# Optimization experiments

Hardware: AMD Instinct MI355X
Metric: run time of the kernel (lower is better)

## Reference

```python
import jax, jax.numpy as jnp
import numpy as np

N_NODES = 20000


def _gcn_conv(x, edge_index, W, b):
    """PyG GCNConv: add self-loops, symmetric normalization, x @ W, scatter-add, + bias."""
    n = x.shape[0]
    loops = jnp.arange(n, dtype=edge_index.dtype)
    src = jnp.concatenate([edge_index[0], loops])  # [E+N]
    dst = jnp.concatenate([edge_index[1], loops])  # [E+N]
    # degree of target nodes (edge weight 1), self-loops guarantee deg >= 1
    deg = jax.ops.segment_sum(jnp.ones_like(dst, dtype=x.dtype), dst, num_segments=n)
    dinv = jax.lax.rsqrt(deg)
    norm = dinv[src] * dinv[dst]  # [E+N]
    h = x @ W  # [n, out] dense GEMM before aggregation (standard GCNConv ordering)
    msg = h[src] * norm[:, None]  # gather + scale over edges
    out = jax.ops.segment_sum(msg, dst, num_segments=n)  # scatter-add to targets
    return out + b


def setup_inputs() -> dict:
    key = jax.random.key(0)
    k = jax.random.split(key, 6)
    in_f, h_f, n_cls = 512, 512, 256
    x = jax.random.normal(k[0], (N_NODES, in_f), dtype=jnp.float32)
    edge_index = jax.random.randint(k[1], (2, 160000), 0, N_NODES, dtype=jnp.int64)
    W1 = jax.random.normal(k[2], (in_f, h_f), dtype=jnp.float32) * (1.0 / np.sqrt(in_f))
    b1 = jnp.zeros((h_f,), dtype=jnp.float32)
    W2 = jax.random.normal(k[3], (h_f, n_cls), dtype=jnp.float32) * (1.0 / np.sqrt(h_f))
    b2 = jnp.zeros((n_cls,), dtype=jnp.float32)
    return {"x": x, "edge_index": edge_index, "W1": W1, "b1": b1, "W2": W2, "b2": b2}


def reference(x, edge_index, W1, b1, W2, b2):
    h = jax.nn.relu(_gcn_conv(x, edge_index, W1, b1))
    h = jax.nn.relu(_gcn_conv(h, edge_index, W2, b2))
    # F.dropout in eval mode is identity; reference is deterministic eval-mode forward
    return h
```

## Files before the change

kernel.cpp:

```cpp
#include <hip/hip_runtime.h>


typedef __bf16 bf16x8 __attribute__((ext_vector_type(8)));
typedef float floatx4 __attribute__((ext_vector_type(4)));
typedef unsigned short ushort_t;
typedef unsigned int uint_t;

#define MAXD 32
#define CAP 40

__device__ inline ushort_t f2bf(float f) {
    unsigned u = __builtin_bit_cast(unsigned, f);
    unsigned r = (u + 0x7FFFu + ((u >> 16) & 1u)) >> 16;
    return (ushort_t)r;
}
__device__ inline float bf_lo(uint_t u) { return __builtin_bit_cast(float, u << 16); }
__device__ inline float bf_hi(uint_t u) { return __builtin_bit_cast(float, u & 0xFFFF0000u); }
__device__ inline uint_t pk2(float lo, float hi) {
    return (uint_t)f2bf(lo) | ((uint_t)f2bf(hi) << 16);
}

__device__ inline void transpose_tile(const float* __restrict__ in,
                                      ushort_t* __restrict__ out,
                                      int K, int N, int k0, int n0,
                                      ushort_t (*tile)[33]) {
    int tx = threadIdx.x & 31, ty = threadIdx.x >> 5;
    for (int r = ty; r < 32; r += 8)
        tile[r][tx] = f2bf(in[(size_t)(k0 + r) * N + n0 + tx]);
    __syncthreads();
    for (int r = ty; r < 32; r += 8)
        out[(size_t)(n0 + r) * K + k0 + tx] = tile[tx][r];
}

__global__ __launch_bounds__(256) void prep_fused(
    const int* __restrict__ src, const int* __restrict__ dst,
    int* __restrict__ deg, int* __restrict__ col_ell,
    int* __restrict__ ovf_cnt, int* __restrict__ ovf, int e, int nb_e,
    const float* __restrict__ x, ushort_t* __restrict__ xb, long xcount, int nb_conv,
    const float* __restrict__ W1, ushort_t* __restrict__ w1t,
    const float* __restrict__ W2, ushort_t* __restrict__ w2t) {
    __shared__ ushort_t tile[32][33];
    int b = blockIdx.x;
    if (b < nb_e) {
        int i = b * 256 + threadIdx.x;
        if (i < e) {
            int s = src[i], d = dst[i];
            int slot = atomicAdd(&deg[d], 1);
            if (slot < MAXD) {
                col_ell[d * MAXD + slot] = s;
            } else {
                int k = atomicAdd(ovf_cnt, 1);
                ovf[2 * k] = d;
                ovf[2 * k + 1] = s;
            }
        }
        return;
    }
    b -= nb_e;
    if (b < nb_conv) {
        long i = ((long)b * 256 + threadIdx.x) * 4;
        if (i < xcount) {
            float4 v = *(const float4*)(x + i);
            ushort4 o = make_ushort4(f2bf(v.x), f2bf(v.y), f2bf(v.z), f2bf(v.w));
            *(ushort4*)(xb + i) = o;
        }
        return;
    }
    b -= nb_conv;
    if (b < 256) {
        transpose_tile(W1, w1t, 512, 512, (b >> 4) * 32, (b & 15) * 32, tile);
        return;
    }
    b -= 256;
    transpose_tile(W2, w2t, 512, 256, (b >> 3) * 32, (b & 7) * 32, tile);
}

__global__ __launch_bounds__(256) void gemm_mfma(
    const ushort_t* __restrict__ A, const ushort_t* __restrict__ BT,
    ushort_t* __restrict__ C,
    int M, int N, int K, int nbx, int gemm_blocks,
    const int* __restrict__ deg, float* __restrict__ dinv_out, int n) {
    __shared__ __align__(16) ushort_t As[8192];
    __shared__ __align__(16) ushort_t Bs[8192];

    if ((int)blockIdx.x >= gemm_blocks) {
        int i = ((int)blockIdx.x - gemm_blocks) * 256 + threadIdx.x;
        if (i < n) dinv_out[i] = 1.0f / sqrtf((float)(deg[i] + 1));
        return;
    }

    const int bx = (int)blockIdx.x % nbx, by = (int)blockIdx.x / nbx;
    const int tid = threadIdx.x;
    const int w = tid >> 6, lane = tid & 63;
    const int q = lane >> 4, ml = lane & 15;
    const int wm = (w >> 1) * 64, wn = (w & 1) * 64;
    const int row0 = by * 128, col0 = bx * 128;

    const int rr = lane >> 3;
    const int gsw = (lane & 7) ^ (rr & 7);
    const ushort_t* ga[4];
    const ushort_t* gb[4];
    ushort_t* la[4];
    ushort_t* lb[4];
#pragma unroll
    for (int rp = 0; rp < 4; rp++) {
        int r = rp * 32 + w * 8 + rr;
        int gra = min(row0 + r, M - 1);
        ga[rp] = A + (size_t)gra * K + gsw * 8;
        gb[rp] = BT + (size_t)(col0 + r) * K + gsw * 8;
        la[rp] = As + rp * 2048 + w * 512;
        lb[rp] = Bs + rp * 2048 + w * 512;
    }

    const int sel = ml & 7;
    int aoff[2][4], boff[2][4];
#pragma unroll
    for (int st = 0; st < 2; st++)
#pragma unroll
        for (int i = 0; i < 4; i++) {
            int g = q + st * 4;
            aoff[st][i] = (wm + i * 16 + ml) * 64 + ((g ^ sel) << 3);
            boff[st][i] = (wn + i * 16 + ml) * 64 + ((g ^ sel) << 3);
        }

    floatx4 acc[4][4];
#pragma unroll
    for (int i = 0; i < 4; i++)
#pragma unroll
        for (int j = 0; j < 4; j++) acc[i][j] = (floatx4)0.0f;

    for (int kt = 0; kt < K; kt += 64) {
#pragma unroll
        for (int rp = 0; rp < 4; rp++) {
            __builtin_amdgcn_global_load_lds(
                (const __attribute__((address_space(1))) unsigned*)ga[rp],
                (__attribute__((address_space(3))) unsigned*)la[rp], 16, 0, 0);
            __builtin_amdgcn_global_load_lds(
                (const __attribute__((address_space(1))) unsigned*)gb[rp],
                (__attribute__((address_space(3))) unsigned*)lb[rp], 16, 0, 0);
            ga[rp] += 64; gb[rp] += 64;
        }
        __syncthreads();
#pragma unroll
        for (int st = 0; st < 2; st++) {
            bf16x8 af[4], bfr[4];
#pragma unroll
            for (int i = 0; i < 4; i++) {
                af[i] = *(const bf16x8*)(As + aoff[st][i]);
                bfr[i] = *(const bf16x8*)(Bs + boff[st][i]);
            }
#pragma unroll
            for (int i = 0; i < 4; i++)
#pragma unroll
                for (int j = 0; j < 4; j++)
                    acc[i][j] = __builtin_amdgcn_mfma_f32_16x16x32_bf16(
                        af[i], bfr[j], acc[i][j], 0, 0, 0);
        }
        __syncthreads();
    }

#pragma unroll
    for (int i = 0; i < 4; i++) {
        int rbase = row0 + wm + i * 16 + q * 4;
#pragma unroll
        for (int j = 0; j < 4; j++) {
            int gc = col0 + wn + j * 16 + ml;
#pragma unroll
            for (int r = 0; r < 4; r++) {
                int gr = rbase + r;
                if (gr < M) C[(size_t)gr * N + gc] = f2bf(acc[i][j][r]);
            }
        }
    }
}

__global__ __launch_bounds__(256) void agg1gemm2(
    const ushort_t* __restrict__ g,
    const ushort_t* __restrict__ BT,
    const int* __restrict__ deg, const int* __restrict__ col_ell,
    const int* __restrict__ ovf_cnt, const int* __restrict__ ovf,
    const float* __restrict__ dinv, const float* __restrict__ b1,
    ushort_t* __restrict__ g2, int M) {
    __shared__ __align__(16) ushort_t As[16 * 64];
    __shared__ __align__(16) ushort_t Bs[256 * 64];
    __shared__ int2  adj_s[16][CAP];
    __shared__ float b1_s[512];
    __shared__ int   cnt_s[16];

    const int tid = threadIdx.x;
    const int w = tid >> 6, lane = tid & 63;
    const int q = lane >> 4, ml = lane & 15;
    const int wn = w * 64;
    const int row0 = (int)blockIdx.x * 16;

    for (int i = tid; i < 512; i += 256) b1_s[i] = b1[i];
    {
        int r = tid >> 4, jj = tid & 15;
        int rg = min(row0 + r, M - 1);
        int cnt = min(deg[rg], MAXD);
        const int* cm = col_ell + (size_t)rg * MAXD;
#pragma unroll
        for (int pass = 0; pass < 3; pass++) {
            int j = jj + pass * 16;
            if (j >= CAP) break;
            int2 a;
            if (j == 0) {
                a.x = rg;
                a.y = __builtin_bit_cast(int, dinv[rg]);
                cnt_s[r] = cnt + 1;
            } else {
                bool vld = (j - 1) < cnt;
                int c = vld ? cm[j - 1] : rg;
                a.x = c;
                a.y = vld ? __builtin_bit_cast(int, dinv[c]) : 0;
            }
            adj_s[r][j] = a;
        }
    }
    const int nov = *ovf_cnt;

    const int rr = lane >> 3;
    const int gsw = (lane & 7) ^ (rr & 7);
    const ushort_t* gb[8];
    ushort_t* lb[8];
#pragma unroll
    for (int rp = 0; rp < 8; rp++) {
        gb[rp] = BT + (size_t)(rp * 32 + w * 8 + rr) * 512 + gsw * 8;
        lb[rp] = Bs + rp * 2048 + w * 512;
    }

    const int sel = ml & 7;
    int aoff[2], boff[2][4];
#pragma unroll
    for (int st = 0; st < 2; st++) {
        int gg = q + st * 4;
        aoff[st] = ml * 64 + ((gg ^ sel) << 3);
#pragma unroll
        for (int i = 0; i < 4; i++)
            boff[st][i] = (wn + i * 16 + ml) * 64 + ((gg ^ sel) << 3);
    }

    floatx4 acc[4];
#pragma unroll
    for (int j = 0; j < 4; j++) acc[j] = (floatx4)0.0f;

    const int gr_ = tid >> 4;
    const int fc = tid & 15;

    __syncthreads();
    const int cntR = cnt_s[gr_];
    const float pdr = __builtin_bit_cast(float, adj_s[gr_][0].y);
    const int selfR = adj_s[gr_][0].x;

    for (int kt = 0; kt < 512; kt += 64) {
#pragma unroll
        for (int rp = 0; rp < 8; rp++) {
            __builtin_amdgcn_global_load_lds(
                (const __attribute__((address_space(1))) unsigned*)gb[rp],
                (__attribute__((address_space(3))) unsigned*)lb[rp], 16, 0, 0);
            gb[rp] += 64;
        }

        const ushort_t* gk = g + kt + fc * 4;
        float a0 = 0.0f, a1 = 0.0f, a2 = 0.0f, a3 = 0.0f;
        for (int e0 = 0; e0 < cntR; e0 += 8) {
            uint2 u[8];
            float ps[8];
#pragma unroll
            for (int j = 0; j < 8; j++) {
                int2 cp = adj_s[gr_][e0 + j];
                ps[j] = __builtin_bit_cast(float, cp.y);
                u[j] = *(const uint2*)(gk + (size_t)cp.x * 512);
            }
#pragma unroll
            for (int j = 0; j < 8; j++) {
                a0 = fmaf(ps[j], bf_lo(u[j].x), a0);
                a1 = fmaf(ps[j], bf_hi(u[j].x), a1);
                a2 = fmaf(ps[j], bf_lo(u[j].y), a2);
                a3 = fmaf(ps[j], bf_hi(u[j].y), a3);
            }
        }
        for (int k2 = 0; k2 < nov; k2++) {
            if (ovf[2 * k2] == selfR) {
                int s = ovf[2 * k2 + 1];
                float ps = dinv[s];
                uint2 u = *(const uint2*)(gk + (size_t)s * 512);
                a0 = fmaf(ps, bf_lo(u.x), a0);
                a1 = fmaf(ps, bf_hi(u.x), a1);
                a2 = fmaf(ps, bf_lo(u.y), a2);
                a3 = fmaf(ps, bf_hi(u.y), a3);
            }
        }
        float4 bv = *(const float4*)(b1_s + kt + fc * 4);
        float h0 = fmaxf(fmaf(pdr, a0, bv.x), 0.0f);
        float h1 = fmaxf(fmaf(pdr, a1, bv.y), 0.0f);
        float h2 = fmaxf(fmaf(pdr, a2, bv.z), 0.0f);
        float h3 = fmaxf(fmaf(pdr, a3, bv.w), 0.0f);
        uint2 U;
        U.x = pk2(h0, h1);
        U.y = pk2(h2, h3);
        *(uint2*)(As + gr_ * 64 + (((fc >> 1) ^ (gr_ & 7)) << 3) + (fc & 1) * 4) = U;

        __syncthreads();

#pragma unroll
        for (int st = 0; st < 2; st++) {
            bf16x8 af = *(const bf16x8*)(As + aoff[st]);
#pragma unroll
            for (int j = 0; j < 4; j++) {
                bf16x8 bfr = *(const bf16x8*)(Bs + boff[st][j]);
                acc[j] = __builtin_amdgcn_mfma_f32_16x16x32_bf16(af, bfr, acc[j],
                                                                 0, 0, 0);
            }
        }
        __syncthreads();
    }

#pragma unroll
    for (int j = 0; j < 4; j++) {
        int gc = wn + j * 16 + ml;
#pragma unroll
        for (int r = 0; r < 4; r++) {
            int lrow = q * 4 + r;
            int grow = row0 + lrow;
            if (grow < M) {
                float pd = __builtin_bit_cast(float, adj_s[lrow][0].y);
                g2[(size_t)grow * 256 + gc] = f2bf(pd * acc[j][r]);
            }
        }
    }
}

__global__ __launch_bounds__(64) void aggregate2(const uint2* __restrict__ g,
                                                 const int* __restrict__ deg,
                                                 const int* __restrict__ col_ell,
                                                 const int* __restrict__ ovf_cnt,
                                                 const int* __restrict__ ovf,
                                                 const float* __restrict__ dinv,
                                                 const float* __restrict__ bias,
                                                 float* __restrict__ out) {
    const int d = blockIdx.x, t = threadIdx.x;
    const int cnt = min(deg[d], MAXD);
    const float pd = dinv[d];
    const size_t base = (size_t)d * 64 + t;
    const int* cm = col_ell + (size_t)d * MAXD;

    int cv = 0;
    float wv = 0.0f;
    if (t < MAXD && t < cnt) {
        cv = cm[t];
        wv = 1.0f;
    }
    float4 b = *(const float4*)(bias + t * 4);

    uint2 us = g[base];
    float a0 = bf_lo(us.x), a1 = bf_hi(us.x);
    float a2 = bf_lo(us.y), a3 = bf_hi(us.y);

    for (int e0 = 0; e0 < cnt; e0 += 8) {
        uint2 u[8];
        float ws[8];
#pragma unroll
        for (int j = 0; j < 8; j++) {
            int s = __shfl(cv, e0 + j);
            ws[j] = __shfl(wv, e0 + j);
            u[j] = g[(size_t)s * 64 + t];
        }
#pragma unroll
        for (int j = 0; j < 8; j++) {
            a0 = fmaf(ws[j], bf_lo(u[j].x), a0);
            a1 = fmaf(ws[j], bf_hi(u[j].x), a1);
            a2 = fmaf(ws[j], bf_lo(u[j].y), a2);
            a3 = fmaf(ws[j], bf_hi(u[j].y), a3);
        }
    }
    int nov = *ovf_cnt;
    for (int k = 0; k < nov; k++) {
        if (ovf[2 * k] == d) {
            uint2 u = g[(size_t)ovf[2 * k + 1] * 64 + t];
            a0 += bf_lo(u.x); a1 += bf_hi(u.x);
            a2 += bf_lo(u.y); a3 += bf_hi(u.y);
        }
    }
    float4 o;
    o.x = fmaxf(fmaf(pd, a0, b.x), 0.0f);
    o.y = fmaxf(fmaf(pd, a1, b.y), 0.0f);
    o.z = fmaxf(fmaf(pd, a2, b.z), 0.0f);
    o.w = fmaxf(fmaf(pd, a3, b.w), 0.0f);
    *(float4*)(out + (size_t)d * 256 + t * 4) = o;
}

extern "C" void kernel_launch(void* const* d_in, const int* in_sizes, int n_in,
                              void* d_out, int out_size, void* d_ws, size_t ws_size,
                              hipStream_t stream) {
    const float* x  = (const float*)d_in[0];
    const int*   ei = (const int*)d_in[1];
    const float* W1 = (const float*)d_in[2];
    const float* b1 = (const float*)d_in[3];
    const float* W2 = (const float*)d_in[4];
    const float* b2 = (const float*)d_in[5];
    float* out = (float*)d_out;

    const int FIN = 512, FH = 512, FOUT = 256;
    const int n = in_sizes[0] / FIN;
    const int e = in_sizes[1] / 2;
    const int* src = ei;
    const int* dst = ei + e;

    auto align_up = [](size_t v) { return (v + 255) & ~(size_t)255; };
    char* w = (char*)d_ws;
    int*      deg     = (int*)w;
    int*      ovf_cnt = deg + n;
    w += align_up((size_t)(n + 1) * 4);
    float*    dinv    = (float*)w;    w += align_up((size_t)n * 4);
    int*      col_ell = (int*)w;      w += align_up((size_t)n * MAXD * 4);
    int*      ovf     = (int*)w;      w += align_up((size_t)2048 * 4);
    ushort_t* xb      = (ushort_t*)w; w += align_up((size_t)n * FIN * 2);
    ushort_t* w1t     = (ushort_t*)w; w += align_up((size_t)FH * FIN * 2);
    ushort_t* w2t     = (ushort_t*)w; w += align_up((size_t)FOUT * FH * 2);
    ushort_t* g       = (ushort_t*)w; w += align_up((size_t)n * FH * 2);
    ushort_t* g2      = (ushort_t*)w; w += align_up((size_t)n * FOUT * 2);

    const int nb_n = (n + 255) / 256;
    const int nb_e = (e + 255) / 256;
    const long xcount = (long)n * FIN;
    const int nb_conv = (int)((xcount / 4 + 255) / 256);

    hipMemsetAsync(deg, 0, (size_t)(n + 1) * 4, stream);

    prep_fused<<<nb_e + nb_conv + 256 + 128, 256, 0, stream>>>(
        src, dst, deg, col_ell, ovf_cnt, ovf, e, nb_e,
        x, xb, xcount, nb_conv, W1, w1t, W2, w2t);

    {
        const int mb = (n + 127) / 128;
        int gemm_blocks = (FH / 128) * mb;
        gemm_mfma<<<gemm_blocks + nb_n, 256, 0, stream>>>(
            xb, w1t, g, n, FH, FIN, FH / 128, gemm_blocks, deg, dinv, n);
    }
    agg1gemm2<<<(n + 15) / 16, 256, 0, stream>>>(
        g, w2t, deg, col_ell, ovf_cnt, ovf, dinv, b1, g2, n);

    aggregate2<<<n, 64, 0, stream>>>((const uint2*)g2, deg, col_ell, ovf_cnt,
                                     ovf, dinv, b2, out);

    (void)ws_size; (void)n_in; (void)out_size;
}
```

Before: 190.6 us.

## Gather full aggregated rows once into LDS before the second-layer GEMM

The fused aggregate+GEMM kernel now handles 32 rows per 512-thread block. Each thread gathers a contiguous 32-element slice of each neighbour's row with 16-byte loads, two edges at a time. The whole 32x512 aggregated, biased and ReLU'd tile is staged in LDS before the MFMA k-loop. This replaces the earlier scheme, which gathered 4 elements per k-tile, 8 edges at a time, inside the GEMM loop. The goal is wider, more coalesced gather traffic and fewer per-tile barriers, at the cost of much more LDS per block, which limits occupancy, and less overlap between the gather and the B-tile loads.

```diff
diff --git a/kernel.cpp b/kernel.cpp
--- a/kernel.cpp
+++ b/kernel.cpp
@@ -7,7 +7,7 @@
 typedef unsigned int uint_t;
 
 #define MAXD 32
-#define CAP 40
+#define CAP 34
 
 __device__ inline ushort_t f2bf(float f) {
     unsigned u = __builtin_bit_cast(unsigned, f);
@@ -174,26 +174,26 @@
     }
 }
 
-__global__ __launch_bounds__(256) void agg1gemm2(
+__global__ __launch_bounds__(512, 4) void agg1gemm2(
     const ushort_t* __restrict__ g,
     const ushort_t* __restrict__ BT,
     const int* __restrict__ deg, const int* __restrict__ col_ell,
     const int* __restrict__ ovf_cnt, const int* __restrict__ ovf,
     const float* __restrict__ dinv, const float* __restrict__ b1,
     ushort_t* __restrict__ g2, int M) {
-    __shared__ __align__(16) ushort_t As[16 * 64];
+    __shared__ __align__(16) ushort_t As[32 * 512];
     __shared__ __align__(16) ushort_t Bs[256 * 64];
-    __shared__ int2  adj_s[16][CAP];
+    __shared__ int2  adj_s[32][CAP];
     __shared__ float b1_s[512];
-    __shared__ int   cnt_s[16];
+    __shared__ int   cnt_s[32];
 
     const int tid = threadIdx.x;
     const int w = tid >> 6, lane = tid & 63;
     const int q = lane >> 4, ml = lane & 15;
-    const int wn = w * 64;
-    const int row0 = (int)blockIdx.x * 16;
-
-    for (int i = tid; i < 512; i += 256) b1_s[i] = b1[i];
+    const int wm = (w >> 2) * 16, wn = (w & 3) * 64;
+    const int row0 = (int)blockIdx.x * 32;
+
+    b1_s[tid] = b1[tid];
     {
         int r = tid >> 4, jj = tid & 15;
         int rg = min(row0 + r, M - 1);
@@ -218,114 +218,159 @@
         }
     }
     const int nov = *ovf_cnt;
+    __syncthreads();
 
     const int rr = lane >> 3;
     const int gsw = (lane & 7) ^ (rr & 7);
-    const ushort_t* gb[8];
-    ushort_t* lb[8];
-#pragma unroll
-    for (int rp = 0; rp < 8; rp++) {
-        gb[rp] = BT + (size_t)(rp * 32 + w * 8 + rr) * 512 + gsw * 8;
-        lb[rp] = Bs + rp * 2048 + w * 512;
-    }
-
-    const int sel = ml & 7;
-    int aoff[2], boff[2][4];
-#pragma unroll
-    for (int st = 0; st < 2; st++) {
-        int gg = q + st * 4;
-        aoff[st] = ml * 64 + ((gg ^ sel) << 3);
-#pragma unroll
-        for (int i = 0; i < 4; i++)
-            boff[st][i] = (wn + i * 16 + ml) * 64 + ((gg ^ sel) << 3);
-    }
-
-    floatx4 acc[4];
-#pragma unroll
-    for (int j = 0; j < 4; j++) acc[j] = (floatx4)0.0f;
-
-    const int gr_ = tid >> 4;
-    const int fc = tid & 15;
-
-    __syncthreads();
-    const int cntR = cnt_s[gr_];
-    const float pdr = __builtin_bit_cast(float, adj_s[gr_][0].y);
-    const int selfR = adj_s[gr_][0].x;
-
-    for (int kt = 0; kt < 512; kt += 64) {
-#pragma unroll
-        for (int rp = 0; rp < 8; rp++) {
-            __builtin_amdgcn_global_load_lds(
-                (const __attribute__((address_space(1))) unsigned*)gb[rp],
-                (__attribute__((address_space(3))) unsigned*)lb[rp], 16, 0, 0);
-            gb[rp] += 64;
-        }
-
-        const ushort_t* gk = g + kt + fc * 4;
-        float a0 = 0.0f, a1 = 0.0f, a2 = 0.0f, a3 = 0.0f;
-        for (int e0 = 0; e0 < cntR; e0 += 8) {
-            uint2 u[8];
-            float ps[8];
-#pragma unroll
-            for (int j = 0; j < 8; j++) {
-                int2 cp = adj_s[gr_][e0 + j];
-                ps[j] = __builtin_bit_cast(float, cp.y);
-                u[j] = *(const uint2*)(gk + (size_t)cp.x * 512);
-            }
-#pragma unroll
-            for (int j = 0; j < 8; j++) {
-                a0 = fmaf(ps[j], bf_lo(u[j].x), a0);
-                a1 = fmaf(ps[j], bf_hi(u[j].x), a1);
-                a2 = fmaf(ps[j], bf_lo(u[j].y), a2);
-                a3 = fmaf(ps[j], bf_hi(u[j].y), a3);
-            }
-        }
-        for (int k2 = 0; k2 < nov; k2++) {
-            if (ovf[2 * k2] == selfR) {
-                int s = ovf[2 * k2 + 1];
-                float ps = dinv[s];
-                uint2 u = *(const uint2*)(gk + (size_t)s * 512);
-                a0 = fmaf(ps, bf_lo(u.x), a0);
-                a1 = fmaf(ps, bf_hi(u.x), a1);
-                a2 = fmaf(ps, bf_lo(u.y), a2);
-                a3 = fmaf(ps, bf_hi(u.y), a3);
-            }
-        }
-        float4 bv = *(const float4*)(b1_s + kt + fc * 4);
-        float h0 = fmaxf(fmaf(pdr, a0, bv.x), 0.0f);
-        float h1 = fmaxf(fmaf(pdr, a1, bv.y), 0.0f);
-        float h2 = fmaxf(fmaf(pdr, a2, bv.z), 0.0f);
-        float h3 = fmaxf(fmaf(pdr, a3, bv.w), 0.0f);
-        uint2 U;
+    const ushort_t* gb[4];
+    ushort_t* lb[4];
+#pragma unroll
+    for (int rp = 0; rp < 4; rp++) {
+        gb[rp] = BT + (size_t)(rp * 64 + w * 8 + rr) * 512 + gsw * 8;
+        lb[rp] = Bs + (rp * 64 + w * 8) * 64;
+    }
+#pragma unroll
+    for (int rp = 0; rp < 4; rp++) {
+        __builtin_amdgcn_global_load_lds(
+            (const __attribute__((address_space(1))) unsigned*)gb[rp],
+            (__attribute__((address_space(3))) unsigned*)lb[rp], 16, 0, 0);
+        gb[rp] += 64;
+    }
+
+    const int r = tid >> 4;
+    const int c = tid & 15;
+    const int cntR = cnt_s[r];
+    const float pdr = __builtin_bit_cast(float, adj_s[r][0].y);
+    const int selfR = adj_s[r][0].x;
+
+    float acc[32];
+#pragma unroll
+    for (int i = 0; i < 32; i++) acc[i] = 0.0f;
+
+    for (int e0 = 0; e0 < cntR; e0 += 2) {
+        int2 cp0 = adj_s[r][e0];
+        int2 cp1 = adj_s[r][e0 + 1];
+        float ps0 = __builtin_bit_cast(float, cp0.y);
+        float ps1 = __builtin_bit_cast(float, cp1.y);
+        const ushort_t* p0 = g + (size_t)cp0.x * 512 + c * 32;
+        const ushort_t* p1 = g + (size_t)cp1.x * 512 + c * 32;
+        uint4 u0[4], u1[4];
+#pragma unroll
+        for (int s = 0; s < 4; s++) u0[s] = *(const uint4*)(p0 + s * 8);
+#pragma unroll
+        for (int s = 0; s < 4; s++) u1[s] = *(const uint4*)(p1 + s * 8);
+#pragma unroll
+        for (int s = 0; s < 4; s++) {
+            acc[s * 8 + 0] = fmaf(ps0, bf_lo(u0[s].x), acc[s * 8 + 0]);
+            acc[s * 8 + 1] = fmaf(ps0, bf_hi(u0[s].x), acc[s * 8 + 1]);
+            acc[s * 8 + 2] = fmaf(ps0, bf_lo(u0[s].y), acc[s * 8 + 2]);
+            acc[s * 8 + 3] = fmaf(ps0, bf_hi(u0[s].y), acc[s * 8 + 3]);
+            acc[s * 8 + 4] = fmaf(ps0, bf_lo(u0[s].z), acc[s * 8 + 4]);
+            acc[s * 8 + 5] = fmaf(ps0, bf_hi(u0[s].z), acc[s * 8 + 5]);
+            acc[s * 8 + 6] = fmaf(ps0, bf_lo(u0[s].w), acc[s * 8 + 6]);
+            acc[s * 8 + 7] = fmaf(ps0, bf_hi(u0[s].w), acc[s * 8 + 7]);
+        }
+#pragma unroll
+        for (int s = 0; s < 4; s++) {
+            acc[s * 8 + 0] = fmaf(ps1, bf_lo(u1[s].x), acc[s * 8 + 0]);
+            acc[s * 8 + 1] = fmaf(ps1, bf_hi(u1[s].x), acc[s * 8 + 1]);
+            acc[s * 8 + 2] = fmaf(ps1, bf_lo(u1[s].y), acc[s * 8 + 2]);
+            acc[s * 8 + 3] = fmaf(ps1, bf_hi(u1[s].y), acc[s * 8 + 3]);
+            acc[s * 8 + 4] = fmaf(ps1, bf_lo(u1[s].z), acc[s * 8 + 4]);
+            acc[s * 8 + 5] = fmaf(ps1, bf_hi(u1[s].z), acc[s * 8 + 5]);
+            acc[s * 8 + 6] = fmaf(ps1, bf_lo(u1[s].w), acc[s * 8 + 6]);
+            acc[s * 8 + 7] = fmaf(ps1, bf_hi(u1[s].w), acc[s * 8 + 7]);
+        }
+    }
+    for (int k2 = 0; k2 < nov; k2++) {
+        if (ovf[2 * k2] == selfR) {
+            int sI = ovf[2 * k2 + 1];
+            float ps = dinv[sI];
+            const ushort_t* p0 = g + (size_t)sI * 512 + c * 32;
+#pragma unroll
+            for (int s = 0; s < 4; s++) {
+                uint4 u = *(const uint4*)(p0 + s * 8);
+                acc[s * 8 + 0] = fmaf(ps, bf_lo(u.x), acc[s * 8 + 0]);
+                acc[s * 8 + 1] = fmaf(ps, bf_hi(u.x), acc[s * 8 + 1]);
+                acc[s * 8 + 2] = fmaf(ps, bf_lo(u.y), acc[s * 8 + 2]);
+                acc[s * 8 + 3] = fmaf(ps, bf_hi(u.y), acc[s * 8 + 3]);
+                acc[s * 8 + 4] = fmaf(ps, bf_lo(u.z), acc[s * 8 + 4]);
+                acc[s * 8 + 5] = fmaf(ps, bf_hi(u.z), acc[s * 8 + 5]);
+                acc[s * 8 + 6] = fmaf(ps, bf_lo(u.w), acc[s * 8 + 6]);
+                acc[s * 8 + 7] = fmaf(ps, bf_hi(u.w), acc[s * 8 + 7]);
+            }
+        }
+    }
+
+#pragma unroll
+    for (int s = 0; s < 4; s++) {
+        float4 b0 = *(const float4*)(b1_s + c * 32 + s * 8);
+        float4 b1v = *(const float4*)(b1_s + c * 32 + s * 8 + 4);
+        float h0 = fmaxf(fmaf(pdr, acc[s * 8 + 0], b0.x), 0.0f);
+        float h1 = fmaxf(fmaf(pdr, acc[s * 8 + 1], b0.y), 0.0f);
+        float h2 = fmaxf(fmaf(pdr, acc[s * 8 + 2], b0.z), 0.0f);
+        float h3 = fmaxf(fmaf(pdr, acc[s * 8 + 3], b0.w), 0.0f);
+        float h4 = fmaxf(fmaf(pdr, acc[s * 8 + 4], b1v.x), 0.0f);
+        float h5 = fmaxf(fmaf(pdr, acc[s * 8 + 5], b1v.y), 0.0f);
+        float h6 = fmaxf(fmaf(pdr, acc[s * 8 + 6], b1v.z), 0.0f);
+        float h7 = fmaxf(fmaf(pdr, acc[s * 8 + 7], b1v.w), 0.0f);
+        uint4 U;
         U.x = pk2(h0, h1);
         U.y = pk2(h2, h3);
-        *(uint2*)(As + gr_ * 64 + (((fc >> 1) ^ (gr_ & 7)) << 3) + (fc & 1) * 4) = U;
-
+        U.z = pk2(h4, h5);
+        U.w = pk2(h6, h7);
+        int gabs = c * 4 + s;
+        int pos = (gabs & ~7) | ((gabs & 7) ^ (r & 7));
+        *(uint4*)(As + r * 512 + pos * 8) = U;
+    }
+
+    const int sel = ml & 7;
+    int aoffb[2], boff[2][4];
+#pragma unroll
+    for (int st = 0; st < 2; st++) {
+        aoffb[st] = (wm + ml) * 512 + (((st * 4 + q) ^ sel) << 3);
+#pragma unroll
+        for (int i = 0; i < 4; i++)
+            boff[st][i] = (wn + i * 16 + ml) * 64 + (((q + st * 4) ^ sel) << 3);
+    }
+    floatx4 accm[4];
+#pragma unroll
+    for (int j = 0; j < 4; j++) accm[j] = (floatx4)0.0f;
+
+    for (int kt = 0; kt < 8; kt++) {
         __syncthreads();
-
 #pragma unroll
         for (int st = 0; st < 2; st++) {
-            bf16x8 af = *(const bf16x8*)(As + aoff[st]);
+            bf16x8 af = *(const bf16x8*)(As + aoffb[st] + kt * 64);
 #pragma unroll
             for (int j = 0; j < 4; j++) {
                 bf16x8 bfr = *(const bf16x8*)(Bs + boff[st][j]);
-                acc[j] = __builtin_amdgcn_mfma_f32_16x16x32_bf16(af, bfr, acc[j],
-                                                                 0, 0, 0);
+                accm[j] = __builtin_amdgcn_mfma_f32_16x16x32_bf16(af, bfr,
+                                                                  accm[j], 0, 0, 0);
             }
         }
         __syncthreads();
+        if (kt < 7) {
+#pragma unroll
+            for (int rp = 0; rp < 4; rp++) {
+                __builtin_amdgcn_global_load_lds(
+                    (const __attribute__((address_space(1))) unsigned*)gb[rp],
+                    (__attribute__((address_space(3))) unsigned*)lb[rp], 16, 0, 0);
+                gb[rp] += 64;
+            }
+        }
     }
 
 #pragma unroll
     for (int j = 0; j < 4; j++) {
         int gc = wn + j * 16 + ml;
 #pragma unroll
-        for (int r = 0; r < 4; r++) {
-            int lrow = q * 4 + r;
+        for (int rg = 0; rg < 4; rg++) {
+            int lrow = wm + q * 4 + rg;
             int grow = row0 + lrow;
             if (grow < M) {
                 float pd = __builtin_bit_cast(float, adj_s[lrow][0].y);
-                g2[(size_t)grow * 256 + gc] = f2bf(pd * acc[j][r]);
+                g2[(size_t)grow * 256 + gc] = f2bf(pd * accm[j][rg]);
             }
         }
     }
@@ -438,7 +483,7 @@
         gemm_mfma<<<gemm_blocks + nb_n, 256, 0, stream>>>(
             xb, w1t, g, n, FH, FIN, FH / 128, gemm_blocks, deg, dinv, n);
     }
-    agg1gemm2<<<(n + 15) / 16, 256, 0, stream>>>(
+    agg1gemm2<<<(n + 31) / 32, 512, 0, stream>>>(
         g, w2t, deg, col_ell, ovf_cnt, ovf, dinv, b1, g2, n);
 
     aggregate2<<<n, 64, 0, stream>>>((const uint2*)g2, deg, col_ell, ovf_cnt,
```

Result: faster. 184.0 us (-3.5%).
